# Kernel tuning notes

Hardware: AMD Instinct MI355X
Metric: run time of the kernel (lower is better)

## Reference

```python
import jax, jax.numpy as jnp
import numpy as np

B, H, W, C = 4, 64, 64, 512
CR = C // 8  # reduced channel dim for query/key (conv_b, conv_c)


def setup_inputs() -> dict:
    key = jax.random.key(0)
    k1, k2, k3, k4, k5 = jax.random.split(key, 5)
    x = jax.random.normal(k1, (B, H, W, C), dtype=jnp.float32)
    # 1x1 conv kernels (no bias) == dense weights applied per pixel
    Wb = jax.random.normal(k2, (C, CR), dtype=jnp.float32) * (2.0 / C) ** 0.5
    Wc = jax.random.normal(k3, (C, CR), dtype=jnp.float32) * (2.0 / C) ** 0.5
    Wd = jax.random.normal(k4, (C, C), dtype=jnp.float32) * (2.0 / C) ** 0.5
    gamma = jax.random.normal(k5, (1,), dtype=jnp.float32)
    return {"x": x, "Wb": Wb, "Wc": Wc, "Wd": Wd, "gamma": gamma}


def reference(x, Wb, Wc, Wd, gamma):
    b, h, w, c = x.shape
    n = h * w
    xf = x.reshape(b, n, c)                       # [B,N,C] flatten spatial
    q = jnp.einsum('bnc,cd->bnd', xf, Wb)         # conv_b: [B,N,CR]
    k = jnp.einsum('bnc,cd->bnd', xf, Wc)         # conv_c: [B,N,CR]
    v = jnp.einsum('bnc,cd->bnd', xf, Wd)         # conv_d: [B,N,C]
    scores = jnp.einsum('bnd,bmd->bnm', q, k)     # [B,N,N] position affinities
    attn = jax.nn.softmax(scores, axis=-1)
    out = jnp.einsum('bnm,bmc->bnc', attn, v)     # [B,N,C]
    out = out.reshape(b, h, w, c)
    return gamma * out + x
```

## Files before the change

kernel.cpp:

```cpp
#include <hip/hip_runtime.h>


typedef __bf16 bf16_t;
typedef __bf16 bf16x8 __attribute__((ext_vector_type(8)));
typedef float f32x4 __attribute__((ext_vector_type(4)));
typedef unsigned long long u64;

#define NN 4096
#define CC 512
#define VSTRIDE 4160u
#define PSTRIDE 4160u
#define ESHIFT 90.0f

#define OFF_QH 0u
#define OFF_QL 1048576u
#define OFF_KH 2097152u
#define OFF_KL 3145728u
#define OFF_VT 4194304u
#define OFF_WBH 29491200u
#define OFF_WBL 29523968u
#define OFF_WCH 29556736u
#define OFF_WCL 29589504u
#define OFF_WD  29622272u
#define OFF_P   12713984u
#define PBATCH  17039360u

static __device__ __forceinline__ f32x4 mfma16(bf16x8 a, bf16x8 b, f32x4 c) {
    return __builtin_amdgcn_mfma_f32_16x16x32_bf16(a, b, c, 0, 0, 0);
}

static __device__ __forceinline__ void load_lds16(const bf16_t* g, bf16_t* l) {
    __builtin_amdgcn_global_load_lds(
        (const __attribute__((address_space(1))) unsigned int*)g,
        (__attribute__((address_space(3))) unsigned int*)l, 16, 0, 0);
}

__global__ __launch_bounds__(256) void prep_kernel(const float* __restrict__ Wb,
                                                   const float* __restrict__ Wc,
                                                   const float* __restrict__ Wd,
                                                   bf16_t* __restrict__ ws) {
    int j = blockIdx.x * 256 + threadIdx.x;
    if (j < 32768) {
        int n = j >> 9, k = j & 511;
        float v = Wb[k * 64 + n];
        bf16_t h = (bf16_t)v;
        ws[OFF_WBH + j] = h;
        ws[OFF_WBL + j] = (bf16_t)(v - (float)h);
    } else if (j < 65536) {
        int j2 = j - 32768;
        int n = j2 >> 9, k = j2 & 511;
        float v = Wc[k * 64 + n];
        bf16_t h = (bf16_t)v;
        ws[OFF_WCH + j2] = h;
        ws[OFF_WCL + j2] = (bf16_t)(v - (float)h);
    } else if (j < 327680) {
        int j2 = j - 65536;
        int n = j2 >> 9, k = j2 & 511;
        ws[OFF_WD + j2] = (bf16_t)Wd[k * 512 + n];
    }
}

__global__ __launch_bounds__(256, 1) void qkv_kernel(const float* __restrict__ x,
                                                     bf16_t* __restrict__ ws) {
    int mt = blockIdx.x;
    int tid = threadIdx.x;
    int w = tid >> 6, lane = tid & 63, quad = lane >> 4, l16 = lane & 15;

    __shared__ __align__(16) bf16_t Vs[64][72];

    const float* xrow = x + (size_t)(mt * 64 + w * 16 + l16) * 512 + quad * 8;
    bf16x8 xh[16], xl[16];
#pragma unroll
    for (int ks = 0; ks < 16; ++ks) {
        f32x4 a0 = *(const f32x4*)(xrow + ks * 32);
        f32x4 a1 = *(const f32x4*)(xrow + ks * 32 + 4);
#pragma unroll
        for (int j = 0; j < 4; ++j) {
            bf16_t h0 = (bf16_t)a0[j];
            bf16_t h1 = (bf16_t)a1[j];
            xh[ks][j] = h0;     xl[ks][j] = (bf16_t)(a0[j] - (float)h0);
            xh[ks][4 + j] = h1; xl[ks][4 + j] = (bf16_t)(a1[j] - (float)h1);
        }
    }

    for (int nT = 0; nT < 2; ++nT) {
        const bf16_t* wh = ws + (nT == 0 ? OFF_WBH : OFF_WCH);
        const bf16_t* wl = ws + (nT == 0 ? OFF_WBL : OFF_WCL);
        f32x4 acc[4];
#pragma unroll
        for (int nt = 0; nt < 4; ++nt) acc[nt] = (f32x4){0.f, 0.f, 0.f, 0.f};
#pragma unroll
        for (int ks = 0; ks < 16; ++ks) {
#pragma unroll
            for (int nt = 0; nt < 4; ++nt) {
                size_t wo = (size_t)(nt * 16 + l16) * 512 + ks * 32 + quad * 8;
                bf16x8 bh = *(const bf16x8*)(wh + wo);
                bf16x8 bl = *(const bf16x8*)(wl + wo);
                acc[nt] = mfma16(xh[ks], bh, acc[nt]);
                acc[nt] = mfma16(xh[ks], bl, acc[nt]);
                acc[nt] = mfma16(xl[ks], bh, acc[nt]);
            }
        }
        unsigned base_h = (nT == 0) ? OFF_QH : OFF_KH;
        unsigned base_l = (nT == 0) ? OFF_QL : OFF_KL;
#pragma unroll
        for (int nt = 0; nt < 4; ++nt) {
            int gc = nt * 16 + l16;
#pragma unroll
            for (int r = 0; r < 4; ++r) {
                int gr = mt * 64 + w * 16 + quad * 4 + r;
                int b = gr >> 12, np = gr & 4095;
                float v = acc[nt][r];
                bf16_t h = (bf16_t)v;
                size_t o = ((size_t)(b * 4096 + np)) * 64 + gc;
                ws[base_h + o] = h;
                ws[base_l + o] = (bf16_t)(v - (float)h);
            }
        }
    }

    for (int nT = 0; nT < 8; ++nT) {
        const bf16_t* wp = ws + OFF_WD + (size_t)nT * 64 * 512;
        f32x4 acc[4];
#pragma unroll
        for (int nt = 0; nt < 4; ++nt) acc[nt] = (f32x4){0.f, 0.f, 0.f, 0.f};
#pragma unroll
        for (int ks = 0; ks < 16; ++ks) {
#pragma unroll
            for (int nt = 0; nt < 4; ++nt) {
                bf16x8 bb = *(const bf16x8*)(wp + (size_t)(nt * 16 + l16) * 512 + ks * 32 + quad * 8);
                acc[nt] = mfma16(xh[ks], bb, acc[nt]);
            }
        }
#pragma unroll
        for (int nt = 0; nt < 4; ++nt) {
            bf16_t pk[4];
#pragma unroll
            for (int r = 0; r < 4; ++r) pk[r] = (bf16_t)acc[nt][r];
            *(u64*)&Vs[nt * 16 + l16][w * 16 + quad * 4] = *(u64*)pk;
        }
        __syncthreads();
        int gr0 = mt * 64;
        int bb = gr0 >> 12, np0 = gr0 & 4095;
        int ch = tid >> 2, seg = tid & 3;
        f32x4 d0 = *(const f32x4*)&Vs[ch][seg * 16];
        f32x4 d1 = *(const f32x4*)&Vs[ch][seg * 16 + 8];
        bf16_t* dst = ws + OFF_VT +
            ((size_t)bb * 512 + (size_t)(nT * 64 + ch)) * VSTRIDE + np0 + seg * 16;
        *(f32x4*)(dst) = d0;
        *(f32x4*)(dst + 8) = d1;
        __syncthreads();
    }
}

__global__ __launch_bounds__(256, 2) void score_kernel(bf16_t* __restrict__ ws) {
    int idx = blockIdx.x;
    int mt = idx & 31;
    int nt = (idx >> 5) & 31;
    int b  = idx >> 10;
    int tid = threadIdx.x;
    int w = tid >> 6, lane = tid & 63, quad = lane >> 4, l16 = lane & 15;
    int wr = w >> 1, wc = w & 1;

    __shared__ __align__(16) bf16_t Ls[128][136];

    const bf16_t* Qh = ws + OFF_QH + (size_t)b * NN * 64;
    const bf16_t* Ql = ws + OFF_QL + (size_t)b * NN * 64;
    const bf16_t* Kh = ws + OFF_KH + (size_t)b * NN * 64;
    const bf16_t* Kl = ws + OFF_KL + (size_t)b * NN * 64;

    bf16x8 qh[4][2], ql[4][2];
#pragma unroll
    for (int rt = 0; rt < 4; ++rt) {
        size_t qo = (size_t)(nt * 128 + wr * 64 + rt * 16 + l16) * 64 + quad * 8;
        qh[rt][0] = *(const bf16x8*)(Qh + qo);
        qh[rt][1] = *(const bf16x8*)(Qh + qo + 32);
        ql[rt][0] = *(const bf16x8*)(Ql + qo);
        ql[rt][1] = *(const bf16x8*)(Ql + qo + 32);
    }

    f32x4 s[4][4];
#pragma unroll
    for (int ct = 0; ct < 4; ++ct) {
        size_t ko = (size_t)(mt * 128 + wc * 64 + ct * 16 + l16) * 64 + quad * 8;
        bf16x8 kh0 = *(const bf16x8*)(Kh + ko);
        bf16x8 kh1 = *(const bf16x8*)(Kh + ko + 32);
        bf16x8 kl0 = *(const bf16x8*)(Kl + ko);
        bf16x8 kl1 = *(const bf16x8*)(Kl + ko + 32);
#pragma unroll
        for (int rt = 0; rt < 4; ++rt) {
            f32x4 a = (f32x4){0.f, 0.f, 0.f, 0.f};
            a = mfma16(qh[rt][0], kh0, a);
            a = mfma16(qh[rt][1], kh1, a);
            a = mfma16(qh[rt][0], kl0, a);
            a = mfma16(qh[rt][1], kl1, a);
            a = mfma16(ql[rt][0], kh0, a);
            a = mfma16(ql[rt][1], kh1, a);
            s[rt][ct] = a;
        }
    }

#pragma unroll
    for (int rt = 0; rt < 4; ++rt)
#pragma unroll
        for (int ct = 0; ct < 4; ++ct)
#pragma unroll
            for (int r = 0; r < 4; ++r) {
                float p = __expf(s[rt][ct][r] - ESHIFT);
                Ls[wr * 64 + rt * 16 + quad * 4 + r][wc * 64 + ct * 16 + l16] = (bf16_t)p;
            }
    __syncthreads();

    bf16_t* P = ws + OFF_P + (size_t)b * PBATCH;
    int row0 = tid >> 4, chunk = tid & 15;
#pragma unroll
    for (int it = 0; it < 8; ++it) {
        int row = it * 16 + row0;
        f32x4 d = *(const f32x4*)&Ls[row][chunk * 8];
        *(f32x4*)(P + (size_t)(nt * 128 + row) * PSTRIDE + mt * 128 + chunk * 8) = d;
    }
}

__global__ __launch_bounds__(256, 2) void pv_kernel(const float* __restrict__ x,
                                                    const float* __restrict__ gamma_p,
                                                    const bf16_t* __restrict__ ws,
                                                    float* __restrict__ out) {
    int idx = blockIdx.x;
    int ct4 = idx & 3;
    int b   = (idx >> 2) & 3;
    int nt  = idx >> 4;
    int tid = threadIdx.x;
    int w = tid >> 6, lane = tid & 63, quad = lane >> 4, l16 = lane & 15;
    int wr = w >> 1, wc = w & 1;

    __shared__ __align__(16) bf16_t Pt_s[4096];
    __shared__ __align__(16) bf16_t Vt_s[4096];
    __shared__ __align__(16) float rsum_s[128];

    const bf16_t* P = ws + OFF_P + (size_t)b * PBATCH + (size_t)(nt * 128) * PSTRIDE;
    const bf16_t* V = ws + OFF_VT + (size_t)b * CC * VSTRIDE + (size_t)(ct4 * 128) * VSTRIDE;

    f32x4 o[4][4];
#pragma unroll
    for (int rt = 0; rt < 4; ++rt)
#pragma unroll
        for (int ct = 0; ct < 4; ++ct) o[rt][ct] = (f32x4){0.f, 0.f, 0.f, 0.f};
    f32x4 osum[4];
#pragma unroll
    for (int rt = 0; rt < 4; ++rt) osum[rt] = (f32x4){0.f, 0.f, 0.f, 0.f};

    bf16_t onev = (bf16_t)1.0f;
    bf16x8 vones = {onev, onev, onev, onev, onev, onev, onev, onev};

    int prow = tid >> 2;
    int pch  = tid & 3;
    const bf16_t* gp0 = P + (size_t)prow * PSTRIDE + pch * 8;
    const bf16_t* gp1 = P + (size_t)(prow + 64) * PSTRIDE + pch * 8;
    const bf16_t* gv0 = V + (size_t)prow * VSTRIDE + pch * 8;
    const bf16_t* gv1 = V + (size_t)(prow + 64) * VSTRIDE + pch * 8;

    for (int k = 0; k < 128; ++k) {
        int m0 = k * 32;
        load_lds16(gp0 + m0, &Pt_s[tid * 8]);
        load_lds16(gp1 + m0, &Pt_s[2048 + tid * 8]);
        load_lds16(gv0 + m0, &Vt_s[tid * 8]);
        load_lds16(gv1 + m0, &Vt_s[2048 + tid * 8]);
        __syncthreads();

        bf16x8 pa[4], vb[4];
#pragma unroll
        for (int rt = 0; rt < 4; ++rt)
            pa[rt] = *(const bf16x8*)&Pt_s[(wr * 64 + rt * 16 + l16) * 32 + quad * 8];
#pragma unroll
        for (int ct = 0; ct < 4; ++ct)
            vb[ct] = *(const bf16x8*)&Vt_s[(wc * 64 + ct * 16 + l16) * 32 + quad * 8];
#pragma unroll
        for (int ct = 0; ct < 4; ++ct)
#pragma unroll
            for (int rt = 0; rt < 4; ++rt)
                o[rt][ct] = mfma16(pa[rt], vb[ct], o[rt][ct]);
        if (wc == 0) {
#pragma unroll
            for (int rt = 0; rt < 4; ++rt) osum[rt] = mfma16(pa[rt], vones, osum[rt]);
        }
        __syncthreads();
    }

    if (wc == 0 && l16 == 0) {
#pragma unroll
        for (int rt = 0; rt < 4; ++rt)
#pragma unroll
            for (int r = 0; r < 4; ++r)
                rsum_s[wr * 64 + rt * 16 + quad * 4 + r] = osum[rt][r];
    }
    __syncthreads();

    float g = gamma_p[0];
#pragma unroll
    for (int rt = 0; rt < 4; ++rt) {
        f32x4 rs = *(const f32x4*)&rsum_s[wr * 64 + rt * 16 + quad * 4];
        f32x4 linv;
#pragma unroll
        for (int r = 0; r < 4; ++r) linv[r] = 1.0f / rs[r];
#pragma unroll
        for (int ct = 0; ct < 4; ++ct) {
#pragma unroll
            for (int r = 0; r < 4; ++r) {
                int n = nt * 128 + wr * 64 + rt * 16 + quad * 4 + r;
                int c = ct4 * 128 + wc * 64 + ct * 16 + l16;
                size_t off = ((size_t)(b * 4096 + n)) * 512 + c;
                out[off] = g * (o[rt][ct][r] * linv[r]) + x[off];
            }
        }
    }
}

extern "C" void kernel_launch(void* const* d_in, const int* in_sizes, int n_in,
                              void* d_out, int out_size, void* d_ws, size_t ws_size,
                              hipStream_t stream) {
    const float* x     = (const float*)d_in[0];
    const float* Wb    = (const float*)d_in[1];
    const float* Wc    = (const float*)d_in[2];
    const float* Wd    = (const float*)d_in[3];
    const float* gamma = (const float*)d_in[4];
    bf16_t* ws = (bf16_t*)d_ws;
    float* out = (float*)d_out;

    prep_kernel<<<1280, 256, 0, stream>>>(Wb, Wc, Wd, ws);
    qkv_kernel<<<256, 256, 0, stream>>>(x, ws);
    score_kernel<<<4096, 256, 0, stream>>>(ws);
    pv_kernel<<<512, 256, 0, stream>>>(x, gamma, ws, out);
}
```

Before: 358.1 us.

## Fuse score and PV kernels into a single flash-style attention kernel

Replaces the separate score kernel, which wrote a full bf16 probability matrix to global memory, and the PV kernel, which read it back, with one fused attention kernel. Each 512-thread block handles 64 query rows across all 512 channels. It computes exp scores per 64-key tile into LDS and immediately multiplies them with V loaded straight from global memory. This removes the large P round trip through HBM, but leaves only 256 blocks, does not stage V through LDS, and recomputes nothing while keeping a fixed exp shift.

```diff
diff --git a/kernel.cpp b/kernel.cpp
--- a/kernel.cpp
+++ b/kernel.cpp
@@ -9,7 +9,6 @@
 #define NN 4096
 #define CC 512
 #define VSTRIDE 4160u
-#define PSTRIDE 4160u
 #define ESHIFT 90.0f
 
 #define OFF_QH 0u
@@ -22,17 +21,9 @@
 #define OFF_WCH 29556736u
 #define OFF_WCL 29589504u
 #define OFF_WD  29622272u
-#define OFF_P   12713984u
-#define PBATCH  17039360u
 
 static __device__ __forceinline__ f32x4 mfma16(bf16x8 a, bf16x8 b, f32x4 c) {
     return __builtin_amdgcn_mfma_f32_16x16x32_bf16(a, b, c, 0, 0, 0);
-}
-
-static __device__ __forceinline__ void load_lds16(const bf16_t* g, bf16_t* l) {
-    __builtin_amdgcn_global_load_lds(
-        (const __attribute__((address_space(1))) unsigned int*)g,
-        (__attribute__((address_space(3))) unsigned int*)l, 16, 0, 0);
 }
 
 __global__ __launch_bounds__(256) void prep_kernel(const float* __restrict__ Wb,
@@ -153,42 +144,55 @@
     }
 }
 
-__global__ __launch_bounds__(256, 2) void score_kernel(bf16_t* __restrict__ ws) {
+__global__ __launch_bounds__(512, 2) void attn_kernel(const float* __restrict__ x,
+                                                      const float* __restrict__ gamma_p,
+                                                      const bf16_t* __restrict__ ws,
+                                                      float* __restrict__ out) {
     int idx = blockIdx.x;
-    int mt = idx & 31;
-    int nt = (idx >> 5) & 31;
-    int b  = idx >> 10;
+    int b = idx & 3;
+    int qt = idx >> 2;
     int tid = threadIdx.x;
     int w = tid >> 6, lane = tid & 63, quad = lane >> 4, l16 = lane & 15;
-    int wr = w >> 1, wc = w & 1;
-
-    __shared__ __align__(16) bf16_t Ls[128][136];
+    int sr = w & 1, sc = w >> 1;
+
+    __shared__ __align__(16) bf16_t Ps[64][72];
 
     const bf16_t* Qh = ws + OFF_QH + (size_t)b * NN * 64;
     const bf16_t* Ql = ws + OFF_QL + (size_t)b * NN * 64;
     const bf16_t* Kh = ws + OFF_KH + (size_t)b * NN * 64;
     const bf16_t* Kl = ws + OFF_KL + (size_t)b * NN * 64;
-
-    bf16x8 qh[4][2], ql[4][2];
-#pragma unroll
-    for (int rt = 0; rt < 4; ++rt) {
-        size_t qo = (size_t)(nt * 128 + wr * 64 + rt * 16 + l16) * 64 + quad * 8;
+    const bf16_t* Vt = ws + OFF_VT + (size_t)b * CC * VSTRIDE;
+
+    bf16x8 qh[2][2], ql[2][2];
+#pragma unroll
+    for (int rt = 0; rt < 2; ++rt) {
+        size_t qo = (size_t)(qt * 64 + sr * 32 + rt * 16 + l16) * 64 + quad * 8;
         qh[rt][0] = *(const bf16x8*)(Qh + qo);
         qh[rt][1] = *(const bf16x8*)(Qh + qo + 32);
         ql[rt][0] = *(const bf16x8*)(Ql + qo);
         ql[rt][1] = *(const bf16x8*)(Ql + qo + 32);
     }
 
-    f32x4 s[4][4];
-#pragma unroll
-    for (int ct = 0; ct < 4; ++ct) {
-        size_t ko = (size_t)(mt * 128 + wc * 64 + ct * 16 + l16) * 64 + quad * 8;
+    f32x4 o[4][4];
+#pragma unroll
+    for (int rt = 0; rt < 4; ++rt)
+#pragma unroll
+        for (int ct = 0; ct < 4; ++ct) o[rt][ct] = (f32x4){0.f, 0.f, 0.f, 0.f};
+    f32x4 osum[4];
+#pragma unroll
+    for (int rt = 0; rt < 4; ++rt) osum[rt] = (f32x4){0.f, 0.f, 0.f, 0.f};
+
+    bf16_t onev = (bf16_t)1.0f;
+    bf16x8 vones = {onev, onev, onev, onev, onev, onev, onev, onev};
+
+    for (int kt = 0; kt < 64; ++kt) {
+        size_t ko = (size_t)(kt * 64 + sc * 16 + l16) * 64 + quad * 8;
         bf16x8 kh0 = *(const bf16x8*)(Kh + ko);
         bf16x8 kh1 = *(const bf16x8*)(Kh + ko + 32);
         bf16x8 kl0 = *(const bf16x8*)(Kl + ko);
         bf16x8 kl1 = *(const bf16x8*)(Kl + ko + 32);
 #pragma unroll
-        for (int rt = 0; rt < 4; ++rt) {
+        for (int rt = 0; rt < 2; ++rt) {
             f32x4 a = (f32x4){0.f, 0.f, 0.f, 0.f};
             a = mfma16(qh[rt][0], kh0, a);
             a = mfma16(qh[rt][1], kh1, a);
@@ -196,118 +200,51 @@
             a = mfma16(qh[rt][1], kl1, a);
             a = mfma16(ql[rt][0], kh0, a);
             a = mfma16(ql[rt][1], kh1, a);
-            s[rt][ct] = a;
-        }
-    }
-
-#pragma unroll
-    for (int rt = 0; rt < 4; ++rt)
-#pragma unroll
-        for (int ct = 0; ct < 4; ++ct)
 #pragma unroll
             for (int r = 0; r < 4; ++r) {
-                float p = __expf(s[rt][ct][r] - ESHIFT);
-                Ls[wr * 64 + rt * 16 + quad * 4 + r][wc * 64 + ct * 16 + l16] = (bf16_t)p;
-            }
-    __syncthreads();
-
-    bf16_t* P = ws + OFF_P + (size_t)b * PBATCH;
-    int row0 = tid >> 4, chunk = tid & 15;
-#pragma unroll
-    for (int it = 0; it < 8; ++it) {
-        int row = it * 16 + row0;
-        f32x4 d = *(const f32x4*)&Ls[row][chunk * 8];
-        *(f32x4*)(P + (size_t)(nt * 128 + row) * PSTRIDE + mt * 128 + chunk * 8) = d;
-    }
-}
-
-__global__ __launch_bounds__(256, 2) void pv_kernel(const float* __restrict__ x,
-                                                    const float* __restrict__ gamma_p,
-                                                    const bf16_t* __restrict__ ws,
-                                                    float* __restrict__ out) {
-    int idx = blockIdx.x;
-    int ct4 = idx & 3;
-    int b   = (idx >> 2) & 3;
-    int nt  = idx >> 4;
-    int tid = threadIdx.x;
-    int w = tid >> 6, lane = tid & 63, quad = lane >> 4, l16 = lane & 15;
-    int wr = w >> 1, wc = w & 1;
-
-    __shared__ __align__(16) bf16_t Pt_s[4096];
-    __shared__ __align__(16) bf16_t Vt_s[4096];
-    __shared__ __align__(16) float rsum_s[128];
-
-    const bf16_t* P = ws + OFF_P + (size_t)b * PBATCH + (size_t)(nt * 128) * PSTRIDE;
-    const bf16_t* V = ws + OFF_VT + (size_t)b * CC * VSTRIDE + (size_t)(ct4 * 128) * VSTRIDE;
-
-    f32x4 o[4][4];
-#pragma unroll
-    for (int rt = 0; rt < 4; ++rt)
-#pragma unroll
-        for (int ct = 0; ct < 4; ++ct) o[rt][ct] = (f32x4){0.f, 0.f, 0.f, 0.f};
-    f32x4 osum[4];
-#pragma unroll
-    for (int rt = 0; rt < 4; ++rt) osum[rt] = (f32x4){0.f, 0.f, 0.f, 0.f};
-
-    bf16_t onev = (bf16_t)1.0f;
-    bf16x8 vones = {onev, onev, onev, onev, onev, onev, onev, onev};
-
-    int prow = tid >> 2;
-    int pch  = tid & 3;
-    const bf16_t* gp0 = P + (size_t)prow * PSTRIDE + pch * 8;
-    const bf16_t* gp1 = P + (size_t)(prow + 64) * PSTRIDE + pch * 8;
-    const bf16_t* gv0 = V + (size_t)prow * VSTRIDE + pch * 8;
-    const bf16_t* gv1 = V + (size_t)(prow + 64) * VSTRIDE + pch * 8;
-
-    for (int k = 0; k < 128; ++k) {
-        int m0 = k * 32;
-        load_lds16(gp0 + m0, &Pt_s[tid * 8]);
-        load_lds16(gp1 + m0, &Pt_s[2048 + tid * 8]);
-        load_lds16(gv0 + m0, &Vt_s[tid * 8]);
-        load_lds16(gv1 + m0, &Vt_s[2048 + tid * 8]);
-        __syncthreads();
-
-        bf16x8 pa[4], vb[4];
-#pragma unroll
-        for (int rt = 0; rt < 4; ++rt)
-            pa[rt] = *(const bf16x8*)&Pt_s[(wr * 64 + rt * 16 + l16) * 32 + quad * 8];
-#pragma unroll
-        for (int ct = 0; ct < 4; ++ct)
-            vb[ct] = *(const bf16x8*)&Vt_s[(wc * 64 + ct * 16 + l16) * 32 + quad * 8];
-#pragma unroll
-        for (int ct = 0; ct < 4; ++ct)
-#pragma unroll
-            for (int rt = 0; rt < 4; ++rt)
-                o[rt][ct] = mfma16(pa[rt], vb[ct], o[rt][ct]);
-        if (wc == 0) {
-#pragma unroll
-            for (int rt = 0; rt < 4; ++rt) osum[rt] = mfma16(pa[rt], vones, osum[rt]);
-        }
-        __syncthreads();
-    }
-
-    if (wc == 0 && l16 == 0) {
-#pragma unroll
-        for (int rt = 0; rt < 4; ++rt)
-#pragma unroll
-            for (int r = 0; r < 4; ++r)
-                rsum_s[wr * 64 + rt * 16 + quad * 4 + r] = osum[rt][r];
-    }
-    __syncthreads();
+                float p = __expf(a[r] - ESHIFT);
+                Ps[sr * 32 + rt * 16 + quad * 4 + r][sc * 16 + l16] = (bf16_t)p;
+            }
+        }
+        __syncthreads();
+
+        bf16x8 pa[4][2];
+#pragma unroll
+        for (int rt = 0; rt < 4; ++rt) {
+            pa[rt][0] = *(const bf16x8*)&Ps[rt * 16 + l16][quad * 8];
+            pa[rt][1] = *(const bf16x8*)&Ps[rt * 16 + l16][32 + quad * 8];
+        }
+#pragma unroll
+        for (int ct = 0; ct < 4; ++ct) {
+            const bf16_t* vrow = Vt + (size_t)(w * 64 + ct * 16 + l16) * VSTRIDE + kt * 64 + quad * 8;
+            bf16x8 v0 = *(const bf16x8*)(vrow);
+            bf16x8 v1 = *(const bf16x8*)(vrow + 32);
+#pragma unroll
+            for (int rt = 0; rt < 4; ++rt) {
+                o[rt][ct] = mfma16(pa[rt][0], v0, o[rt][ct]);
+                o[rt][ct] = mfma16(pa[rt][1], v1, o[rt][ct]);
+            }
+        }
+#pragma unroll
+        for (int rt = 0; rt < 4; ++rt) {
+            osum[rt] = mfma16(pa[rt][0], vones, osum[rt]);
+            osum[rt] = mfma16(pa[rt][1], vones, osum[rt]);
+        }
+        __syncthreads();
+    }
 
     float g = gamma_p[0];
 #pragma unroll
     for (int rt = 0; rt < 4; ++rt) {
-        f32x4 rs = *(const f32x4*)&rsum_s[wr * 64 + rt * 16 + quad * 4];
         f32x4 linv;
 #pragma unroll
-        for (int r = 0; r < 4; ++r) linv[r] = 1.0f / rs[r];
+        for (int r = 0; r < 4; ++r) linv[r] = 1.0f / osum[rt][r];
 #pragma unroll
         for (int ct = 0; ct < 4; ++ct) {
 #pragma unroll
             for (int r = 0; r < 4; ++r) {
-                int n = nt * 128 + wr * 64 + rt * 16 + quad * 4 + r;
-                int c = ct4 * 128 + wc * 64 + ct * 16 + l16;
+                int n = qt * 64 + rt * 16 + quad * 4 + r;
+                int c = w * 64 + ct * 16 + l16;
                 size_t off = ((size_t)(b * 4096 + n)) * 512 + c;
                 out[off] = g * (o[rt][ct][r] * linv[r]) + x[off];
             }
@@ -328,6 +265,5 @@
 
     prep_kernel<<<1280, 256, 0, stream>>>(Wb, Wc, Wd, ws);
     qkv_kernel<<<256, 256, 0, stream>>>(x, ws);
-    score_kernel<<<4096, 256, 0, stream>>>(ws);
-    pv_kernel<<<512, 256, 0, stream>>>(x, gamma, ws, out);
-}
+    attn_kernel<<<256, 512, 0, stream>>>(x, gamma, ws, out);
+}
```

After: 425.3 us. +18.8%, slower.
